# Kernel optimization log

Measured on AMD Instinct MI355X. Metric: run time of the kernel, lower is better.

Reference implementation:

```python
import jax, jax.numpy as jnp
import numpy as np

EPS = 1e-6
TAU = 0.07


def setup_inputs() -> dict:
    key = jax.random.key(0)
    kx, ky = jax.random.split(key)
    B, D = 4096, 1024
    x = jax.random.normal(kx, (B, D), dtype=jnp.float32)
    y = jax.random.normal(ky, (B, D), dtype=jnp.float32)
    return {"x": x, "y": y}


def reference(x, y):
    B = x.shape[0]
    # torch CosineSimilarity: dot / (max(||x||, eps) * max(||y||, eps))
    xn = x / jnp.maximum(jnp.linalg.norm(x, axis=-1, keepdims=True), EPS)
    yn = y / jnp.maximum(jnp.linalg.norm(y, axis=-1, keepdims=True), EPS)
    S = jnp.einsum('id,jd->ij', xn, yn)          # [B, B] cosine sims, S[i,j]=cos(x_i,y_j)
    E = jnp.exp(S / TAU)                          # bounded: |S|<=1 so exp <= e^{1/0.07}
    diag = jnp.diagonal(E)
    # original: sum_j (exp + eps) + eps  ->  sum_j exp + B*eps + eps
    extra = B * EPS + EPS
    row_denom = jnp.sum(E, axis=1) + extra        # x->y direction (loop 1)
    col_denom = jnp.sum(E, axis=0) + extra        # y->x direction (loop 2)
    coef = -1.0 / (2.0 * B)
    loss = coef * (jnp.sum(jnp.log(diag / row_denom)) + jnp.sum(jnp.log(diag / col_denom)))
    return loss
```

## Files before the change

kernel.cpp:

```cpp
#include <hip/hip_runtime.h>

#define NB 4096
#define DK 1024
#define EPSF 1e-6f
#define QS 32.0f

typedef __attribute__((ext_vector_type(8))) int   i32x8_t;
typedef __attribute__((ext_vector_type(4))) int   i32x4_t;
typedef __attribute__((ext_vector_type(4))) float f32x4_t;

#if defined(__has_builtin)
#if __has_builtin(__builtin_amdgcn_cvt_scalef32_pk_fp4_f32)
#define HW_FP4 1
#endif
#endif


__device__ __forceinline__ void async16(const void* g, void* lds) {
    __builtin_amdgcn_global_load_lds(
        (const __attribute__((address_space(1))) void*)g,
        (__attribute__((address_space(3))) void*)lds, 16, 0, 0);
}

__device__ __forceinline__ unsigned enc4(float v) {
    const float a = fabsf(v);
    unsigned c = (a >= 0.25f) + (a >= 0.75f) + (a >= 1.25f) + (a >= 1.75f)
               + (a >= 2.5f)  + (a >= 3.5f)  + (a >= 5.0f);
    return c | ((v < 0.f) ? 8u : 0u);
}

__global__ __launch_bounds__(256) void normalize_rows(
    const float* __restrict__ x, const float* __restrict__ y,
    unsigned char* __restrict__ xq, unsigned char* __restrict__ yq,
    float* __restrict__ sdiag, float* __restrict__ zerobuf)
{
    const int t = threadIdx.x;
    const int gid = blockIdx.x * 256 + t;
    if (gid < 2 * NB) zerobuf[gid] = 0.f;
    if (gid == 0) *((unsigned*)(zerobuf + 3 * NB)) = 0u;

    const int wave = t >> 6;
    const int lane = t & 63;
    const int row  = blockIdx.x * 4 + wave;

    const float4* xr = reinterpret_cast<const float4*>(x + (size_t)row * DK);
    const float4* yr = reinterpret_cast<const float4*>(y + (size_t)row * DK);

    float4 xv[4], yv[4];
    float ssx = 0.f, ssy = 0.f, sxy = 0.f;
    #pragma unroll
    for (int jj = 0; jj < 4; ++jj) {
        xv[jj] = xr[lane * 4 + jj];
        yv[jj] = yr[lane * 4 + jj];
        ssx += xv[jj].x*xv[jj].x + xv[jj].y*xv[jj].y + xv[jj].z*xv[jj].z + xv[jj].w*xv[jj].w;
        ssy += yv[jj].x*yv[jj].x + yv[jj].y*yv[jj].y + yv[jj].z*yv[jj].z + yv[jj].w*yv[jj].w;
        sxy += xv[jj].x*yv[jj].x + xv[jj].y*yv[jj].y + xv[jj].z*yv[jj].z + xv[jj].w*yv[jj].w;
    }
    #pragma unroll
    for (int off = 1; off < 64; off <<= 1) {
        ssx += __shfl_xor(ssx, off, 64);
        ssy += __shfl_xor(ssy, off, 64);
        sxy += __shfl_xor(sxy, off, 64);
    }
    const float invx = 1.0f / fmaxf(sqrtf(ssx), EPSF);
    const float invy = 1.0f / fmaxf(sqrtf(ssy), EPSF);
    const float sx = invx * QS;
    const float sy = invy * QS;

    float fx[16], fy[16];
    #pragma unroll
    for (int jj = 0; jj < 4; ++jj) {
        fx[jj*4+0] = xv[jj].x; fx[jj*4+1] = xv[jj].y;
        fx[jj*4+2] = xv[jj].z; fx[jj*4+3] = xv[jj].w;
        fy[jj*4+0] = yv[jj].x; fy[jj*4+1] = yv[jj].y;
        fy[jj*4+2] = yv[jj].z; fy[jj*4+3] = yv[jj].w;
    }

    unsigned xb0, xb1, yb0, yb1;
#ifdef HW_FP4
    #define CVT8(dst, f, s)                                                        \
        dst = __builtin_amdgcn_cvt_scalef32_pk_fp4_f32(0u,  (f)[0]*(s), (f)[1]*(s), 1.0f, 0); \
        dst = __builtin_amdgcn_cvt_scalef32_pk_fp4_f32(dst, (f)[2]*(s), (f)[3]*(s), 1.0f, 1); \
        dst = __builtin_amdgcn_cvt_scalef32_pk_fp4_f32(dst, (f)[4]*(s), (f)[5]*(s), 1.0f, 2); \
        dst = __builtin_amdgcn_cvt_scalef32_pk_fp4_f32(dst, (f)[6]*(s), (f)[7]*(s), 1.0f, 3)
    CVT8(xb0, fx,     sx);
    CVT8(xb1, fx + 8, sx);
    CVT8(yb0, fy,     sy);
    CVT8(yb1, fy + 8, sy);
    #undef CVT8
#else
    unsigned xb[2] = {0u, 0u}, yb[2] = {0u, 0u};
    #pragma unroll
    for (int j = 0; j < 16; ++j) {
        xb[j >> 3] |= enc4(fx[j] * sx) << ((j & 7) * 4);
        yb[j >> 3] |= enc4(fy[j] * sy) << ((j & 7) * 4);
    }
    xb0 = xb[0]; xb1 = xb[1]; yb0 = yb[0]; yb1 = yb[1];
#endif

    const int p = row >> 4, r = row & 15;
    const unsigned off = (unsigned)p * 8192 + (lane >> 3) * 1024 + r * 64
                       + ((((lane & 7) >> 1) ^ (r & 3)) << 4) + (lane & 1) * 8;
    *reinterpret_cast<uint2*>(xq + off) = make_uint2(xb0, xb1);
    *reinterpret_cast<uint2*>(yq + off) = make_uint2(yb0, yb1);

    if (lane == 0) sdiag[row] = sxy * invx * invy;
}

__global__ __launch_bounds__(512) void gemm_exp_sums(
    const unsigned char* __restrict__ xq, const unsigned char* __restrict__ yq,
    float* __restrict__ rowsum, float* __restrict__ colsum,
    const float* __restrict__ sdiag, unsigned* __restrict__ donecnt,
    float* __restrict__ out)
{
    __shared__ __align__(16) unsigned char LDS[2][32768];
    __shared__ unsigned lastFlag;
    __shared__ double dred[8];

    const int t    = threadIdx.x;
    const int lane = t & 63;
    const int wave = t >> 6;
    const int q    = lane >> 4;
    const int l15  = lane & 15;

    const int R0 = blockIdx.y * 256;
    const int C0 = blockIdx.x * 256;
    const int wRow = (wave >> 2) * 64;
    const int wCol = (wave & 3) * 64;

    f32x4_t acc[2][4][4];
    #pragma unroll
    for (int hh = 0; hh < 2; hh++)
        #pragma unroll
        for (int i = 0; i < 4; i++)
            #pragma unroll
            for (int j = 0; j < 4; j++)
                acc[hh][i][j] = (f32x4_t){0.f, 0.f, 0.f, 0.f};

    const unsigned char* srcA =
        xq + (size_t)((R0 >> 4) + 2 * wave) * 8192 + lane * 16;
    const unsigned char* srcB =
        yq + (size_t)((C0 >> 4) + 2 * wave) * 8192 + lane * 16;

    const int sl = (q ^ (l15 & 3)) << 4;

    auto issue = [&](int kb, int buf) {
        #pragma unroll
        for (int pp = 0; pp < 2; ++pp) {
            async16(srcA + pp * 8192 + kb * 1024,
                    &LDS[buf][(2 * wave + pp) * 1024]);
            async16(srcB + pp * 8192 + kb * 1024,
                    &LDS[buf][16384 + (2 * wave + pp) * 1024]);
        }
    };

    issue(0, 0);

    #pragma unroll 1
    for (int kb = 0; kb < 8; ++kb) {
        const int buf = kb & 1;
        if (kb < 7) {
            issue(kb + 1, buf ^ 1);
            __builtin_amdgcn_s_waitcnt(0xF74);
        } else {
            __builtin_amdgcn_s_waitcnt(0xF70);
        }
        __builtin_amdgcn_s_barrier();

        i32x8_t bfr[4];
        #pragma unroll
        for (int nt = 0; nt < 4; ++nt) {
            const i32x4_t v = *reinterpret_cast<const i32x4_t*>(
                &LDS[buf][16384 + ((wCol >> 4) + nt) * 1024 + l15 * 64 + sl]);
            bfr[nt][0] = v[0]; bfr[nt][1] = v[1]; bfr[nt][2] = v[2]; bfr[nt][3] = v[3];
            bfr[nt][4] = 0;    bfr[nt][5] = 0;    bfr[nt][6] = 0;    bfr[nt][7] = 0;
        }
        #pragma unroll
        for (int hh = 0; hh < 2; ++hh) {
            #pragma unroll
            for (int mt = 0; mt < 4; ++mt) {
                const i32x4_t v = *reinterpret_cast<const i32x4_t*>(
                    &LDS[buf][((wRow >> 4) + hh * 8 + mt) * 1024 + l15 * 64 + sl]);
                i32x8_t af;
                af[0] = v[0]; af[1] = v[1]; af[2] = v[2]; af[3] = v[3];
                af[4] = 0;    af[5] = 0;    af[6] = 0;    af[7] = 0;
                #pragma unroll
                for (int nt = 0; nt < 4; ++nt)
                    acc[hh][mt][nt] = __builtin_amdgcn_mfma_scale_f32_16x16x128_f8f6f4(
                        af, bfr[nt], acc[hh][mt][nt],
                        4, 4,
                        0, 0x7F7F7F7F,
                        0, 0x7F7F7F7F);
            }
        }

        __builtin_amdgcn_s_barrier();
    }

    const float kScale = (float)(1.0 / (1024.0 * 0.07 * 0.6931471805599453));
    float csum[4] = {0.f, 0.f, 0.f, 0.f};
    #pragma unroll
    for (int hh = 0; hh < 2; ++hh) {
        #pragma unroll
        for (int mt = 0; mt < 4; ++mt) {
            float rsum[4] = {0.f, 0.f, 0.f, 0.f};
            #pragma unroll
            for (int nt = 0; nt < 4; ++nt) {
                #pragma unroll
                for (int r = 0; r < 4; ++r) {
                    const float e = exp2f(acc[hh][mt][nt][r] * kScale);
                    rsum[r]  += e;
                    csum[nt] += e;
                }
            }
            #pragma unroll
            for (int r = 0; r < 4; ++r) {
                float v = rsum[r];
                v += __shfl_xor(v, 1, 64);
                v += __shfl_xor(v, 2, 64);
                v += __shfl_xor(v, 4, 64);
                v += __shfl_xor(v, 8, 64);
                if (l15 == 0)
                    atomicAdd(&rowsum[R0 + wRow + hh * 128 + mt * 16 + q * 4 + r], v);
            }
        }
    }
    #pragma unroll
    for (int nt = 0; nt < 4; ++nt) {
        float v = csum[nt];
        v += __shfl_xor(v, 16, 64);
        v += __shfl_xor(v, 32, 64);
        if (lane < 16)
            atomicAdd(&colsum[C0 + wCol + nt * 16 + l15], v);
    }

    __syncthreads();
    if (t == 0) {
        __threadfence();
        const unsigned old = __hip_atomic_fetch_add(
            donecnt, 1u, __ATOMIC_ACQ_REL, __HIP_MEMORY_SCOPE_AGENT);
        lastFlag = (old == 255u) ? 1u : 0u;
    }
    __syncthreads();
    if (lastFlag) {
        const float extra = (float)(NB * 1e-6 + 1e-6);
        double local = 0.0;
        for (int i = t; i < NB; i += 512) {
            const float rs = __hip_atomic_load(&rowsum[i], __ATOMIC_RELAXED,
                                               __HIP_MEMORY_SCOPE_AGENT);
            const float cs = __hip_atomic_load(&colsum[i], __ATOMIC_RELAXED,
                                               __HIP_MEMORY_SCOPE_AGENT);
            local += (double)sdiag[i] * (2.0 / 0.07)
                   - (double)logf(rs + extra)
                   - (double)logf(cs + extra);
        }
        #pragma unroll
        for (int off = 1; off < 64; off <<= 1)
            local += __shfl_xor(local, off, 64);
        if ((t & 63) == 0) dred[t >> 6] = local;
        __syncthreads();
        if (t == 0) {
            double tot = 0.0;
            #pragma unroll
            for (int w = 0; w < 8; ++w) tot += dred[w];
            out[0] = (float)(tot * (-1.0 / (2.0 * NB)));
        }
    }
}

extern "C" void kernel_launch(void* const* d_in, const int* in_sizes, int n_in,
                              void* d_out, int out_size, void* d_ws, size_t ws_size,
                              hipStream_t stream)
{
    const float* x = (const float*)d_in[0];
    const float* y = (const float*)d_in[1];
    float* out = (float*)d_out;

    char* ws = (char*)d_ws;
    unsigned char* xq = (unsigned char*)ws;
    unsigned char* yq = (unsigned char*)(ws + (size_t)2 * 1024 * 1024);
    float* rowsum = (float*)(ws + (size_t)8 * 1024 * 1024);
    float* colsum = rowsum + NB;
    float* sdiag  = colsum + NB;
    unsigned* donecnt = (unsigned*)(sdiag + NB);

    normalize_rows<<<NB / 4, 256, 0, stream>>>(x, y, xq, yq, sdiag, rowsum);

    dim3 grid(16, 16);
    gemm_exp_sums<<<grid, 512, 0, stream>>>(xq, yq, rowsum, colsum,
                                            sdiag, donecnt, out);
}
```

Measured before the change: 104.2 us.

## Halve GEMM row tile, triple-buffer LDS, and raise occupancy to 4 blocks

The row tile of the fused GEMM+exp kernel shrinks from 256 to 128, so the grid doubles to 512 blocks and the accumulator registers per thread halve. LDS becomes a three-stage ring with two k-blocks prefetched ahead, and launch_bounds asks for 4 blocks per CU. The aim is to fill all CUs on the 256-CU part, cut register pressure, and hide more load latency. In exchange, B tiles are reloaded twice as often and there are twice as many atomic row and column updates.

```diff
diff --git a/kernel.cpp b/kernel.cpp
--- a/kernel.cpp
+++ b/kernel.cpp
@@ -107,13 +107,13 @@
     if (lane == 0) sdiag[row] = sxy * invx * invy;
 }
 
-__global__ __launch_bounds__(512) void gemm_exp_sums(
+__global__ __launch_bounds__(512, 4) void gemm_exp_sums(
     const unsigned char* __restrict__ xq, const unsigned char* __restrict__ yq,
     float* __restrict__ rowsum, float* __restrict__ colsum,
     const float* __restrict__ sdiag, unsigned* __restrict__ donecnt,
     float* __restrict__ out)
 {
-    __shared__ __align__(16) unsigned char LDS[2][32768];
+    __shared__ __align__(16) unsigned char LDS[3][24576];
     __shared__ unsigned lastFlag;
     __shared__ double dred[8];
 
@@ -123,71 +123,70 @@
     const int q    = lane >> 4;
     const int l15  = lane & 15;
 
-    const int R0 = blockIdx.y * 256;
+    const int R0 = blockIdx.y * 128;
     const int C0 = blockIdx.x * 256;
     const int wRow = (wave >> 2) * 64;
     const int wCol = (wave & 3) * 64;
 
-    f32x4_t acc[2][4][4];
-    #pragma unroll
-    for (int hh = 0; hh < 2; hh++)
-        #pragma unroll
-        for (int i = 0; i < 4; i++)
-            #pragma unroll
-            for (int j = 0; j < 4; j++)
-                acc[hh][i][j] = (f32x4_t){0.f, 0.f, 0.f, 0.f};
+    f32x4_t acc[4][4];
+    #pragma unroll
+    for (int i = 0; i < 4; i++)
+        #pragma unroll
+        for (int j = 0; j < 4; j++)
+            acc[i][j] = (f32x4_t){0.f, 0.f, 0.f, 0.f};
 
     const unsigned char* srcA =
-        xq + (size_t)((R0 >> 4) + 2 * wave) * 8192 + lane * 16;
+        xq + (size_t)((R0 >> 4) + wave) * 8192 + lane * 16;
     const unsigned char* srcB =
         yq + (size_t)((C0 >> 4) + 2 * wave) * 8192 + lane * 16;
 
     const int sl = (q ^ (l15 & 3)) << 4;
 
     auto issue = [&](int kb, int buf) {
-        #pragma unroll
-        for (int pp = 0; pp < 2; ++pp) {
-            async16(srcA + pp * 8192 + kb * 1024,
-                    &LDS[buf][(2 * wave + pp) * 1024]);
+        async16(srcA + kb * 1024, &LDS[buf][wave * 1024]);
+        #pragma unroll
+        for (int pp = 0; pp < 2; ++pp)
             async16(srcB + pp * 8192 + kb * 1024,
-                    &LDS[buf][16384 + (2 * wave + pp) * 1024]);
-        }
+                    &LDS[buf][8192 + (2 * wave + pp) * 1024]);
     };
 
     issue(0, 0);
+    issue(1, 1);
 
     #pragma unroll 1
     for (int kb = 0; kb < 8; ++kb) {
-        const int buf = kb & 1;
-        if (kb < 7) {
-            issue(kb + 1, buf ^ 1);
-            __builtin_amdgcn_s_waitcnt(0xF74);
+        const int buf = kb % 3;
+        if (kb < 6) {
+            issue(kb + 2, (kb + 2) % 3);
+            __builtin_amdgcn_s_waitcnt(0xF76);
+        } else if (kb == 6) {
+            __builtin_amdgcn_s_waitcnt(0xF73);
         } else {
             __builtin_amdgcn_s_waitcnt(0xF70);
         }
         __builtin_amdgcn_s_barrier();
 
-        i32x8_t bfr[4];
-        #pragma unroll
-        for (int nt = 0; nt < 4; ++nt) {
-            const i32x4_t v = *reinterpret_cast<const i32x4_t*>(
-                &LDS[buf][16384 + ((wCol >> 4) + nt) * 1024 + l15 * 64 + sl]);
-            bfr[nt][0] = v[0]; bfr[nt][1] = v[1]; bfr[nt][2] = v[2]; bfr[nt][3] = v[3];
-            bfr[nt][4] = 0;    bfr[nt][5] = 0;    bfr[nt][6] = 0;    bfr[nt][7] = 0;
-        }
-        #pragma unroll
-        for (int hh = 0; hh < 2; ++hh) {
+        #pragma unroll
+        for (int nth = 0; nth < 2; ++nth) {
+            i32x8_t bfr[2];
+            #pragma unroll
+            for (int ni = 0; ni < 2; ++ni) {
+                const i32x4_t v = *reinterpret_cast<const i32x4_t*>(
+                    &LDS[buf][8192 + ((wCol >> 4) + nth * 2 + ni) * 1024 + l15 * 64 + sl]);
+                bfr[ni][0] = v[0]; bfr[ni][1] = v[1]; bfr[ni][2] = v[2]; bfr[ni][3] = v[3];
+                bfr[ni][4] = 0;    bfr[ni][5] = 0;    bfr[ni][6] = 0;    bfr[ni][7] = 0;
+            }
             #pragma unroll
             for (int mt = 0; mt < 4; ++mt) {
                 const i32x4_t v = *reinterpret_cast<const i32x4_t*>(
-                    &LDS[buf][((wRow >> 4) + hh * 8 + mt) * 1024 + l15 * 64 + sl]);
+                    &LDS[buf][((wRow >> 4) + mt) * 1024 + l15 * 64 + sl]);
                 i32x8_t af;
                 af[0] = v[0]; af[1] = v[1]; af[2] = v[2]; af[3] = v[3];
                 af[4] = 0;    af[5] = 0;    af[6] = 0;    af[7] = 0;
                 #pragma unroll
-                for (int nt = 0; nt < 4; ++nt)
-                    acc[hh][mt][nt] = __builtin_amdgcn_mfma_scale_f32_16x16x128_f8f6f4(
-                        af, bfr[nt], acc[hh][mt][nt],
+                for (int ni = 0; ni < 2; ++ni)
+                    acc[mt][nth * 2 + ni] = __builtin_amdgcn_mfma_scale_f32_16x16x128_f8f6f4(
+                        af, bfr[ni], acc[mt][nth * 2 + ni],
                         4, 4,
                         0, 0x7F7F7F7F,
                         0, 0x7F7F7F7F);
@@ -200,29 +199,26 @@
     const float kScale = (float)(1.0 / (1024.0 * 0.07 * 0.6931471805599453));
     float csum[4] = {0.f, 0.f, 0.f, 0.f};
     #pragma unroll
-    for (int hh = 0; hh < 2; ++hh) {
-        #pragma unroll
-        for (int mt = 0; mt < 4; ++mt) {
-            float rsum[4] = {0.f, 0.f, 0.f, 0.f};
-            #pragma unroll
-            for (int nt = 0; nt < 4; ++nt) {
-                #pragma unroll
-                for (int r = 0; r < 4; ++r) {
-                    const float e = exp2f(acc[hh][mt][nt][r] * kScale);
-                    rsum[r]  += e;
-                    csum[nt] += e;
-                }
+    for (int mt = 0; mt < 4; ++mt) {
+        float rsum[4] = {0.f, 0.f, 0.f, 0.f};
+        #pragma unroll
+        for (int nt = 0; nt < 4; ++nt) {
+            #pragma unroll
+            for (int r = 0; r < 4; ++r) {
+                const float e = exp2f(acc[mt][nt][r] * kScale);
+                rsum[r]  += e;
+                csum[nt] += e;
             }
-            #pragma unroll
-            for (int r = 0; r < 4; ++r) {
-                float v = rsum[r];
-                v += __shfl_xor(v, 1, 64);
-                v += __shfl_xor(v, 2, 64);
-                v += __shfl_xor(v, 4, 64);
-                v += __shfl_xor(v, 8, 64);
-                if (l15 == 0)
-                    atomicAdd(&rowsum[R0 + wRow + hh * 128 + mt * 16 + q * 4 + r], v);
-            }
+        }
+        #pragma unroll
+        for (int r = 0; r < 4; ++r) {
+            float v = rsum[r];
+            v += __shfl_xor(v, 1, 64);
+            v += __shfl_xor(v, 2, 64);
+            v += __shfl_xor(v, 4, 64);
+            v += __shfl_xor(v, 8, 64);
+            if (l15 == 0)
+                atomicAdd(&rowsum[R0 + wRow + mt * 16 + q * 4 + r], v);
         }
     }
     #pragma unroll
@@ -239,7 +235,7 @@
         __threadfence();
         const unsigned old = __hip_atomic_fetch_add(
             donecnt, 1u, __ATOMIC_ACQ_REL, __HIP_MEMORY_SCOPE_AGENT);
-        lastFlag = (old == 255u) ? 1u : 0u;
+        lastFlag = (old == 511u) ? 1u : 0u;
     }
     __syncthreads();
     if (lastFlag) {
@@ -286,7 +282,7 @@
 
     normalize_rows<<<NB / 4, 256, 0, stream>>>(x, y, xq, yq, sdiag, rowsum);
 
-    dim3 grid(16, 16);
+    dim3 grid(16, 32);
     gemm_exp_sums<<<grid, 512, 0, stream>>>(xq, yq, rowsum, colsum,
                                             sdiag, donecnt, out);
 }
```

Result: no change. 105.7 us (+1.4%).
